# Kernel optimization log

Measured on AMD Instinct MI355X. Metric: run time of the kernel, lower is better.

Reference implementation:

```python
import jax, jax.numpy as jnp
import numpy as np

C = 128

def setup_inputs() -> dict:
    key = jax.random.key(0)
    ks = jax.random.split(key, 7)
    s = 1.0 / np.sqrt(C)
    return {
        "x": jax.random.normal(ks[0], (8, C, 64, 64), dtype=jnp.float32),
        "Wq": jax.random.uniform(ks[1], (C, C), jnp.float32, -s, s),
        "bq": jax.random.uniform(ks[2], (C,), jnp.float32, -s, s),
        "Wk": jax.random.uniform(ks[3], (C, C), jnp.float32, -s, s),
        "bk": jax.random.uniform(ks[4], (C,), jnp.float32, -s, s),
        "Wv": jax.random.uniform(ks[5], (C, C), jnp.float32, -s, s),
        "bv": jax.random.uniform(ks[6], (C,), jnp.float32, -s, s),
    }

def reference(x, Wq, bq, Wk, bk, Wv, bv):
    bs, c, h, w = x.shape
    xf = x.reshape(bs, c, h * w)                      # [B, C, N]
    # 1x1 convs == per-pixel linear maps over channels
    q = jnp.einsum("dc,bcn->bdn", Wq, xf) + bq[None, :, None]
    k = jnp.einsum("dc,bcn->bdn", Wk, xf) + bk[None, :, None]
    v = jnp.einsum("dc,bcn->bdn", Wv, xf) + bv[None, :, None]
    # energy[b,i,j] = <q[:,i], k[:,j]>  (no 1/sqrt(d) scaling, per original)
    energy = jnp.einsum("bci,bcj->bij", q, k)         # [B, N, N]
    attn = jax.nn.softmax(energy, axis=-1)
    # out[b,c,i] = sum_j v[b,c,j] * attn[b,i,j]
    out = jnp.einsum("bcj,bij->bci", v, attn)
    return out.reshape(bs, c, h, w)
```

## Files before the change

kernel.cpp:

```cpp
#include <hip/hip_runtime.h>
#include <stdint.h>
#include <math.h>

typedef float  f32x4  __attribute__((ext_vector_type(4)));
typedef float  f32x16 __attribute__((ext_vector_type(16)));
typedef short  bf16x8 __attribute__((ext_vector_type(8)));
typedef unsigned int u32;
typedef unsigned int u32x4 __attribute__((ext_vector_type(4)));
typedef unsigned short ushort_t;

#define MFMA32(a, b, c) __builtin_amdgcn_mfma_f32_32x32x16_bf16((a), (b), (c), 0, 0, 0)

constexpr int B_ = 8, C_ = 128, N_ = 4096;
constexpr float LOG2E = 1.44269504088896340736f;

__device__ __forceinline__ u32 pack2bf(float a, float b) {
  u32 ua = __builtin_bit_cast(u32, a);
  u32 ub = __builtin_bit_cast(u32, b);
  ua += 0x7fffu + ((ua >> 16) & 1u);
  ub += 0x7fffu + ((ub >> 16) & 1u);
  return (ua >> 16) | (ub & 0xffff0000u);
}
__device__ __forceinline__ u32 pkfast(float a, float b) {
  u32 ua = __builtin_bit_cast(u32, a) + 0x8000u;
  u32 ub = __builtin_bit_cast(u32, b) + 0x8000u;
  return __builtin_amdgcn_perm(ub, ua, 0x07060302u);
}
__device__ __forceinline__ bf16x8 pack8(const float* v, float s) {
  u32x4 d = { pack2bf(v[0]*s, v[1]*s), pack2bf(v[2]*s, v[3]*s),
              pack2bf(v[4]*s, v[5]*s), pack2bf(v[6]*s, v[7]*s) };
  return __builtin_bit_cast(bf16x8, d);
}

__device__ __forceinline__ bf16x8 mk_pa(const f32x16& sv, int rb, float& lacc) {
  float e0 = __builtin_amdgcn_exp2f(sv[rb+0]);
  float e1 = __builtin_amdgcn_exp2f(sv[rb+1]);
  float e2 = __builtin_amdgcn_exp2f(sv[rb+2]);
  float e3 = __builtin_amdgcn_exp2f(sv[rb+3]);
  float e4 = __builtin_amdgcn_exp2f(sv[rb+4]);
  float e5 = __builtin_amdgcn_exp2f(sv[rb+5]);
  float e6 = __builtin_amdgcn_exp2f(sv[rb+6]);
  float e7 = __builtin_amdgcn_exp2f(sv[rb+7]);
  lacc += ((e0+e1)+(e2+e3)) + ((e4+e5)+(e6+e7));
  u32 a  = pkfast(e0, e1), b2 = pkfast(e2, e3);
  u32 c2 = pkfast(e4, e5), d2 = pkfast(e6, e7);
  asm("v_permlane32_swap_b32 %0, %1" : "+v"(a), "+v"(c2));
  asm("v_permlane32_swap_b32 %0, %1" : "+v"(b2), "+v"(d2));
  u32x4 fr = { a, b2, c2, d2 };
  return __builtin_bit_cast(bf16x8, fr);
}

__global__ __launch_bounds__(256)
void wprep_kernel(const float* __restrict__ Wq, const float* __restrict__ Wk,
                  const float* __restrict__ Wv, ushort_t* __restrict__ Wf)
{
  const int tid  = blockIdx.x * 256 + threadIdx.x;
  const int widx = tid >> 11;
  const int r    = tid & 2047;
  const int dt   = r >> 9;
  const int kc   = (r >> 6) & 7;
  const int ln   = r & 63;
  const float* W = (widx == 0) ? Wq : (widx == 1) ? Wk : Wv;
  const float s  = (widx == 0) ? LOG2E : 1.0f;
  const int d    = dt * 32 + (ln & 31);
  const int c0   = kc * 16 + (ln >> 5) * 8;
  const float* p = W + d * C_ + c0;
  f32x4 lo = *(const f32x4*)p, hi = *(const f32x4*)(p + 4);
  float v[8] = { lo.x, lo.y, lo.z, lo.w, hi.x, hi.y, hi.z, hi.w };
  *(bf16x8*)(Wf + (size_t)tid * 8) = pack8(v, s);
}

__global__ __launch_bounds__(256, 3)
void proj_kernel(const float* __restrict__ x,
                 const float* __restrict__ bq, const float* __restrict__ bk,
                 const float* __restrict__ bv, const ushort_t* __restrict__ Wf,
                 ushort_t* __restrict__ Qf, ushort_t* __restrict__ Kf,
                 ushort_t* __restrict__ Vf)
{
  const int b   = blockIdx.x & 7;
  const int nt  = blockIdx.x >> 3;
  const int n0  = nt << 5;
  const int t   = threadIdx.x;
  const int dt  = t >> 6;
  const int lane = t & 63;
  const int l31 = t & 31;
  const int lq1 = (t >> 5) & 1;

  __shared__ float xs[128 * 33];
  {
    const float* xb = x + (size_t)b * C_ * N_ + n0;
    const int m  = t & 7;
    const int cb = t >> 3;
#pragma unroll
    for (int it = 0; it < 4; ++it) {
      const int c = it * 32 + cb;
      f32x4 v = *(const f32x4*)(xb + (size_t)c * N_ + m * 4);
      *(f32x4*)&xs[c * 33 + m * 4] = v;
    }
  }
  __syncthreads();

  bf16x8 xf[8];
#pragma unroll
  for (int kc = 0; kc < 8; ++kc) {
    float v[8];
#pragma unroll
    for (int e = 0; e < 8; ++e)
      v[e] = xs[(kc * 16 + lq1 * 8 + e) * 33 + l31];
    xf[kc] = pack8(v, 1.0f);
  }

  const ushort_t* WQf = Wf;
  const ushort_t* WKf = Wf + 16384;
  const ushort_t* WVf = Wf + 32768;
  const f32x16 Z = {0,0,0,0,0,0,0,0,0,0,0,0,0,0,0,0};

  f32x16 sq = Z, sk = Z, sv = Z;
#pragma unroll
  for (int kc = 0; kc < 8; ++kc) {
    const size_t wo = (size_t)(dt * 8 + kc) * 512 + lane * 8;
    bf16x8 wq = *(const bf16x8*)(WQf + wo);
    bf16x8 wk = *(const bf16x8*)(WKf + wo);
    bf16x8 wvv = *(const bf16x8*)(WVf + wo);
    sq = MFMA32(wq, xf[kc], sq);
    sk = MFMA32(wk, xf[kc], sk);
    sv = MFMA32(xf[kc], wvv, sv);
  }

#pragma unroll
  for (int q = 0; q < 4; ++q) {
    const int dbase = dt * 32 + q * 8 + lq1 * 4;
    f32x4 b4q = *(const f32x4*)(bq + dbase);
    f32x4 b4k = *(const f32x4*)(bk + dbase);
    uint2 qs, ks;
    qs.x = pack2bf(sq[4*q+0] + b4q.x * LOG2E, sq[4*q+1] + b4q.y * LOG2E);
    qs.y = pack2bf(sq[4*q+2] + b4q.z * LOG2E, sq[4*q+3] + b4q.w * LOG2E);
    ks.x = pack2bf(sk[4*q+0] + b4k.x, sk[4*q+1] + b4k.y);
    ks.y = pack2bf(sk[4*q+2] + b4k.z, sk[4*q+3] + b4k.w);
    const int kcf = dt * 2 + (q >> 1), h = q & 1;
    const size_t off = ((size_t)((b * 128 + nt) * 8 + kcf) * 64 + h * 32 + l31) * 8 + lq1 * 4;
    *(uint2*)(Qf + off) = qs;
    *(uint2*)(Kf + off) = ks;
  }

  {
    const float bvl = bv[dt * 32 + l31];
    const int j64 = nt >> 1, qp = nt & 1;
#pragma unroll
    for (int q = 0; q < 4; ++q) {
      uint2 vs;
      vs.x = pack2bf(sv[4*q+0] + bvl, sv[4*q+1] + bvl);
      vs.y = pack2bf(sv[4*q+2] + bvl, sv[4*q+3] + bvl);
      const int cc = qp * 2 + (q >> 1);
      const size_t off = ((size_t)((b * 64 + j64) * 4 + dt) * 4 + cc) * 512 +
                         (size_t)((q & 1) * 32 + l31) * 8 + lq1 * 4;
      *(uint2*)(Vf + off) = vs;
    }
  }
}

__global__ __launch_bounds__(256, 2)
void flash_kernel(const ushort_t* __restrict__ Qf, const ushort_t* __restrict__ Kf,
                  const ushort_t* __restrict__ Vf, float* __restrict__ out,
                  float* __restrict__ opart, float* __restrict__ lpart, int js)
{
  const int b     = blockIdx.x & 7;
  const int itile = (blockIdx.x >> 3) & 31;
  const int jsl   = blockIdx.x >> 8;
  const int t     = threadIdx.x;
  const int wv    = t >> 6;
  const int lane  = t & 63;
  const int l31   = t & 31;
  const int lq1   = (t >> 5) & 1;
  const int i0    = itile * 128 + wv * 32;

  const int jt0 = (jsl * 128) / js;
  const int jt1 = ((jsl + 1) * 128) / js;
  const ushort_t* Kt0   = Kf + (size_t)b * 524288;
  const ushort_t* Vbase = Vf + (size_t)b * 524288;

  bf16x8 qf[8];
  const size_t qb = (size_t)((b * 128 + itile * 4 + wv) * 8) * 512;
#pragma unroll
  for (int kc = 0; kc < 8; ++kc)
    qf[kc] = *(const bf16x8*)(Qf + qb + (size_t)kc * 512 + lane * 8);

  const f32x16 Z = {0,0,0,0,0,0,0,0,0,0,0,0,0,0,0,0};
  f32x16 o[4] = {Z, Z, Z, Z};
  float lsum = 0.f;

  auto ldK = [&](int jt, bf16x8* kf) {
    const ushort_t* src = Kt0 + (size_t)jt * 4096 + lane * 8;
#pragma unroll
    for (int kc = 0; kc < 8; ++kc)
      kf[kc] = *(const bf16x8*)(src + kc * 512);
  };

  auto body = [&](const bf16x8* kf, int jt) {
    f32x16 s = Z;
#pragma unroll
    for (int kc = 0; kc < 8; ++kc)
      s = MFMA32(kf[kc], qf[kc], s);
    bf16x8 vf[8];
    {
      const ushort_t* src = Vbase + (size_t)(jt >> 1) * 8192 +
                            (size_t)(jt & 1) * 1024 + lane * 8;
#pragma unroll
      for (int ct = 0; ct < 4; ++ct) {
        vf[ct*2+0] = *(const bf16x8*)(src + (ct*4+0) * 512);
        vf[ct*2+1] = *(const bf16x8*)(src + (ct*4+1) * 512);
      }
    }
    bf16x8 pa0 = mk_pa(s, 0, lsum);
    bf16x8 pa1 = mk_pa(s, 8, lsum);
#pragma unroll
    for (int ct = 0; ct < 4; ++ct) {
      o[ct] = MFMA32(vf[ct*2+0], pa0, o[ct]);
      o[ct] = MFMA32(vf[ct*2+1], pa1, o[ct]);
    }
  };

  bf16x8 kfA[8], kfB[8];
  ldK(jt0, kfA);
  for (int n = jt0; n < jt1; n += 2) {
    if (n + 1 < jt1) ldK(n + 1, kfB);
    body(kfA, n);
    if (n + 1 < jt1) {
      if (n + 2 < jt1) ldK(n + 2, kfA);
      body(kfB, n + 1);
    }
  }

  lsum += __shfl_xor(lsum, 32);
  const int ib = i0 + l31;

  if (js == 1) {
    const float inv = 1.0f / lsum;
#pragma unroll
    for (int ct = 0; ct < 4; ++ct)
#pragma unroll
      for (int rg = 0; rg < 16; ++rg) {
        const int c = ct * 32 + (rg >> 2) * 8 + lq1 * 4 + (rg & 3);
        out[(size_t)(b * C_ + c) * N_ + ib] = o[ct][rg] * inv;
      }
  } else {
    float* op = jsl ? (opart + (size_t)(jsl - 1) * B_ * C_ * N_) : out;
#pragma unroll
    for (int ct = 0; ct < 4; ++ct)
#pragma unroll
      for (int rg = 0; rg < 16; ++rg) {
        const int c = ct * 32 + (rg >> 2) * 8 + lq1 * 4 + (rg & 3);
        op[(size_t)(b * C_ + c) * N_ + ib] = o[ct][rg];
      }
    if (lane < 32)
      lpart[(size_t)jsl * B_ * N_ + (size_t)b * N_ + ib] = lsum;
  }
}

__global__ __launch_bounds__(256)
void combine_kernel(const float* __restrict__ opart, const float* __restrict__ lpart,
                    float* __restrict__ out, int js)
{
  const int t  = blockIdx.x * 256 + threadIdx.x;
  const int n4 = (t & 1023) * 4;
  const int bc = t >> 10;
  const int b  = bc >> 7;
  const size_t off  = (size_t)bc * N_ + n4;
  const size_t loff = (size_t)b * N_ + n4;
  f32x4 os = *(const f32x4*)(out + off);
  f32x4 ls = *(const f32x4*)(lpart + loff);
  for (int s = 1; s < js; ++s) {
    os += *(const f32x4*)(opart + (size_t)(s - 1) * B_ * C_ * N_ + off);
    ls += *(const f32x4*)(lpart + (size_t)s * B_ * N_ + loff);
  }
  f32x4 r = { os.x / ls.x, os.y / ls.y, os.z / ls.z, os.w / ls.w };
  *(f32x4*)(out + off) = r;
}

extern "C" void kernel_launch(void* const* d_in, const int* in_sizes, int n_in,
                              void* d_out, int out_size, void* d_ws, size_t ws_size,
                              hipStream_t stream) {
  const float* x  = (const float*)d_in[0];
  const float* Wq = (const float*)d_in[1];
  const float* bq = (const float*)d_in[2];
  const float* Wk = (const float*)d_in[3];
  const float* bk = (const float*)d_in[4];
  const float* Wv = (const float*)d_in[5];
  const float* bv = (const float*)d_in[6];
  float* out = (float*)d_out;

  const size_t nc = (size_t)B_ * N_ * C_;
  ushort_t* qf = (ushort_t*)d_ws;
  ushort_t* kf = qf + nc;
  ushort_t* vf = kf + nc;
  ushort_t* wf = vf + nc;
  const size_t base = (3 * nc + 49152) * sizeof(ushort_t);

  auto need = [&](int jss) {
    return base + (size_t)jss * (size_t)B_ * N_ * 4 +
           (size_t)(jss - 1) * (size_t)B_ * C_ * N_ * 4;
  };
  const int js = (ws_size >= need(2)) ? 2 : 1;

  float* lpart = (float*)((char*)d_ws + base);
  float* opart = lpart + (size_t)js * B_ * N_;

  hipLaunchKernelGGL(wprep_kernel, dim3(24), dim3(256), 0, stream, Wq, Wk, Wv, wf);
  hipLaunchKernelGGL(proj_kernel, dim3(1024), dim3(256), 0, stream,
                     x, bq, bk, bv, wf, qf, kf, vf);
  hipLaunchKernelGGL(flash_kernel, dim3(256 * js), dim3(256), 0, stream,
                     qf, kf, vf, out, opart, lpart, js);
  if (js > 1)
    hipLaunchKernelGGL(combine_kernel, dim3(4096), dim3(256), 0, stream,
                       opart, lpart, out, js);
}
```

Before: 175.9 us.

## Stage K tiles through LDS with async triple buffering and raise occupancy

K tiles for the flash kernel are now copied straight from global memory into a triple-buffered LDS ring using global_load_lds, two tiles ahead, with workgroup barriers between iterations, instead of being double-buffered in registers per wave. This frees registers, so launch bounds rise to 3 blocks per SM, and s_setprio is set around the MFMA sections. The key split factor can also go to 3 when the workspace allows it. The aim is to share K loads across the four waves of a block and hide their latency. In exchange it adds per-iteration barriers and more combine work.

```diff
diff --git a/kernel.cpp b/kernel.cpp
--- a/kernel.cpp
+++ b/kernel.cpp
@@ -30,6 +30,12 @@
   u32x4 d = { pack2bf(v[0]*s, v[1]*s), pack2bf(v[2]*s, v[3]*s),
               pack2bf(v[4]*s, v[5]*s), pack2bf(v[6]*s, v[7]*s) };
   return __builtin_bit_cast(bf16x8, d);
+}
+
+__device__ __forceinline__ void gload_lds16(const ushort_t* g, ushort_t* l) {
+  __builtin_amdgcn_global_load_lds(
+      (const __attribute__((address_space(1))) void*)g,
+      (__attribute__((address_space(3))) void*)l, 16, 0, 0);
 }
 
 __device__ __forceinline__ bf16x8 mk_pa(const f32x16& sv, int rb, float& lacc) {
@@ -159,7 +165,7 @@
   }
 }
 
-__global__ __launch_bounds__(256, 2)
+__global__ __launch_bounds__(256, 3)
 void flash_kernel(const ushort_t* __restrict__ Qf, const ushort_t* __restrict__ Kf,
                   const ushort_t* __restrict__ Vf, float* __restrict__ out,
                   float* __restrict__ opart, float* __restrict__ lpart, int js)
@@ -174,60 +180,85 @@
   const int lq1   = (t >> 5) & 1;
   const int i0    = itile * 128 + wv * 32;
 
+  __shared__ __align__(16) short smem[12288];
+
   const int jt0 = (jsl * 128) / js;
   const int jt1 = ((jsl + 1) * 128) / js;
+  const int NT  = jt1 - jt0;
   const ushort_t* Kt0   = Kf + (size_t)b * 524288;
   const ushort_t* Vbase = Vf + (size_t)b * 524288;
 
+  auto stageK = [&](int jt, int p) {
+    ushort_t* buf = (ushort_t*)smem + p * 4096;
+    const ushort_t* src = Kt0 + (size_t)jt * 4096;
+#pragma unroll
+    for (int c = 0; c < 2; ++c) {
+      const int g = wv * 2 + c;
+      gload_lds16(src + g * 512 + lane * 8, buf + g * 512);
+    }
+  };
+
   bf16x8 qf[8];
   const size_t qb = (size_t)((b * 128 + itile * 4 + wv) * 8) * 512;
 #pragma unroll
   for (int kc = 0; kc < 8; ++kc)
     qf[kc] = *(const bf16x8*)(Qf + qb + (size_t)kc * 512 + lane * 8);
+
+  stageK(jt0, 0);
+  stageK(jt0 + 1, 1);
+  asm volatile("s_waitcnt vmcnt(2)" ::: "memory");
+  __builtin_amdgcn_sched_barrier(0);
+  __builtin_amdgcn_s_barrier();
+  __builtin_amdgcn_sched_barrier(0);
 
   const f32x16 Z = {0,0,0,0,0,0,0,0,0,0,0,0,0,0,0,0};
   f32x16 o[4] = {Z, Z, Z, Z};
   float lsum = 0.f;
 
-  auto ldK = [&](int jt, bf16x8* kf) {
-    const ushort_t* src = Kt0 + (size_t)jt * 4096 + lane * 8;
-#pragma unroll
-    for (int kc = 0; kc < 8; ++kc)
-      kf[kc] = *(const bf16x8*)(src + kc * 512);
-  };
-
-  auto body = [&](const bf16x8* kf, int jt) {
-    f32x16 s = Z;
-#pragma unroll
-    for (int kc = 0; kc < 8; ++kc)
-      s = MFMA32(kf[kc], qf[kc], s);
+  int pcur = 0, pstage = 2;
+  for (int n = 0; n < NT; ++n) {
+    const int jt = jt0 + n;
+
     bf16x8 vf[8];
     {
-      const ushort_t* src = Vbase + (size_t)(jt >> 1) * 8192 +
-                            (size_t)(jt & 1) * 1024 + lane * 8;
+      const ushort_t* vsrc = Vbase + (size_t)(jt >> 1) * 8192 +
+                             (size_t)(jt & 1) * 1024 + lane * 8;
 #pragma unroll
       for (int ct = 0; ct < 4; ++ct) {
-        vf[ct*2+0] = *(const bf16x8*)(src + (ct*4+0) * 512);
-        vf[ct*2+1] = *(const bf16x8*)(src + (ct*4+1) * 512);
+        vf[ct*2+0] = *(const bf16x8*)(vsrc + (ct*4+0) * 512);
+        vf[ct*2+1] = *(const bf16x8*)(vsrc + (ct*4+1) * 512);
       }
     }
+    __builtin_amdgcn_sched_barrier(0);
+
+    if (n + 2 < NT) stageK(jt0 + n + 2, pstage);
+    pstage = (pstage == 2) ? 0 : pstage + 1;
+    const short* kb = smem + pcur * 4096;
+    pcur = (pcur == 2) ? 0 : pcur + 1;
+
+    __builtin_amdgcn_s_setprio(1);
+    f32x16 s = Z;
+#pragma unroll
+    for (int kc = 0; kc < 8; ++kc) {
+      bf16x8 kfr = *(const bf16x8*)&kb[kc * 512 + lane * 8];
+      s = MFMA32(kfr, qf[kc], s);
+    }
+    __builtin_amdgcn_s_setprio(0);
     bf16x8 pa0 = mk_pa(s, 0, lsum);
     bf16x8 pa1 = mk_pa(s, 8, lsum);
+    __builtin_amdgcn_s_setprio(1);
 #pragma unroll
     for (int ct = 0; ct < 4; ++ct) {
       o[ct] = MFMA32(vf[ct*2+0], pa0, o[ct]);
       o[ct] = MFMA32(vf[ct*2+1], pa1, o[ct]);
     }
-  };
-
-  bf16x8 kfA[8], kfB[8];
-  ldK(jt0, kfA);
-  for (int n = jt0; n < jt1; n += 2) {
-    if (n + 1 < jt1) ldK(n + 1, kfB);
-    body(kfA, n);
-    if (n + 1 < jt1) {
-      if (n + 2 < jt1) ldK(n + 2, kfA);
-      body(kfB, n + 1);
+    __builtin_amdgcn_s_setprio(0);
+
+    if (n + 1 < NT) {
+      asm volatile("s_waitcnt vmcnt(2)" ::: "memory");
+      __builtin_amdgcn_sched_barrier(0);
+      __builtin_amdgcn_s_barrier();
+      __builtin_amdgcn_sched_barrier(0);
     }
   }
 
@@ -300,7 +331,7 @@
     return base + (size_t)jss * (size_t)B_ * N_ * 4 +
            (size_t)(jss - 1) * (size_t)B_ * C_ * N_ * 4;
   };
-  const int js = (ws_size >= need(2)) ? 2 : 1;
+  const int js = (ws_size >= need(3)) ? 3 : (ws_size >= need(2)) ? 2 : 1;
 
   float* lpart = (float*)((char*)d_ws + base);
   float* opart = lpart + (size_t)js * B_ * N_;
```

After: 174.6 us. No clear change (-0.7%).
